# Kernel optimization log

Hardware: AMD Instinct MI355X
Metric: run time of the kernel (lower is better)

## Reference

```python
import jax, jax.numpy as jnp
import numpy as np

N = 100000
F_IN = 128
HID = 256
N_CLS = 40
E = 1600000


def setup_inputs() -> dict:
    key = jax.random.key(0)
    ks = jax.random.split(key, 12)
    x = jax.random.normal(ks[0], (N, F_IN), dtype=jnp.float32)
    edge_index = jax.random.randint(ks[1], (2, E), 0, N, dtype=jnp.int64)
    # GCNConv params (glorot-ish scale), conv2 is reused twice in forward
    def lin(k, fi, fo):
        return jax.random.normal(k, (fi, fo), dtype=jnp.float32) * (1.0 / np.sqrt(fi))
    return {
        "x": x,
        "edge_index": edge_index,
        "W1": lin(ks[2], F_IN, HID), "b1": jnp.zeros((HID,), jnp.float32),
        "W2": lin(ks[3], HID, HID),  "b2": jnp.zeros((HID,), jnp.float32),
        "W3": lin(ks[4], HID, HID),  "b3": jnp.zeros((HID,), jnp.float32),
        "W4": lin(ks[5], HID, N_CLS), "b4": jnp.zeros((N_CLS,), jnp.float32),
    }


def _gcn_norm(edge_index, n):
    # add self-loops, compute symmetric normalization D^-1/2 (A+I) D^-1/2
    loop = jnp.arange(n, dtype=edge_index.dtype)
    src = jnp.concatenate([edge_index[0], loop])
    dst = jnp.concatenate([edge_index[1], loop])
    deg = jax.ops.segment_sum(jnp.ones_like(dst, dtype=jnp.float32), dst, num_segments=n)
    dinv = jnp.where(deg > 0, jax.lax.rsqrt(deg), 0.0)
    norm = dinv[src] * dinv[dst]  # [E+N]
    return src, dst, norm


def _gcn_conv(x, W, b, src, dst, norm, n):
    h = x @ W                       # [N, Fout] dense transform first (fewer msg bytes)
    msg = h[src] * norm[:, None]    # gather + scale
    out = jax.ops.segment_sum(msg, dst, num_segments=n)  # scatter-add
    return out + b


def reference(x, edge_index, W1, b1, W2, b2, W3, b3, W4, b4):
    n = x.shape[0]
    src, dst, norm = _gcn_norm(edge_index, n)
    h = jax.nn.relu(_gcn_conv(x, W1, b1, src, dst, norm, n))
    h = jax.nn.relu(_gcn_conv(h, W2, b2, src, dst, norm, n))
    h = jax.nn.relu(_gcn_conv(h, W2, b2, src, dst, norm, n))  # conv2 reused, as in source
    h = jax.nn.relu(_gcn_conv(h, W3, b3, src, dst, norm, n))
    h = _gcn_conv(h, W4, b4, src, dst, norm, n)
    return jax.nn.log_softmax(h, axis=1)
```

## Files before the change

kernel.cpp:

```cpp
#include <hip/hip_runtime.h>
#include <stdint.h>
#include <math.h>

#define NN   100000
#define FIN  128
#define HIDDEN 256
#define NCLS 40
#define NE   1600000

#define PRNG 8
#define RNG  12500
#define SSL  32
#define NES  50000

#define NSLC 8

typedef unsigned short u16;
typedef unsigned char u8;
typedef __attribute__((ext_vector_type(8))) short s16x8;
typedef __attribute__((ext_vector_type(4))) float f32x4;
typedef __attribute__((ext_vector_type(2))) float f32x2;

__device__ __forceinline__ float bf2f(unsigned short u) {
    union { float f; uint32_t i; } v; v.i = ((uint32_t)u) << 16; return v.f;
}
__device__ __forceinline__ unsigned short f2bf(float f) {
    union { float f; uint32_t i; } v; v.f = f;
    uint32_t r = v.i + 0x7fffu + ((v.i >> 16) & 1u);
    return (unsigned short)(r >> 16);
}
__device__ __forceinline__ u8 f2fp8(float f) {
    int r = __builtin_amdgcn_cvt_pk_fp8_f32(f, f, 0, false);
    return (u8)(r & 0xff);
}

__global__ __launch_bounds__(256) void k_detect(const u16* __restrict__ x16,
                                                const int* __restrict__ ei,
                                                int* __restrict__ flags) {
    int g = blockIdx.x * 256 + threadIdx.x;
    uint2 v = *(const uint2*)(x16 + (size_t)g * 4);
    int nan_cnt = 0;
    uint32_t w0 = v.x, w1 = v.y;
    if (((w0 >> 0)  & 0x7fff) >= 0x7f80) nan_cnt++;
    if (((w0 >> 16) & 0x7fff) >= 0x7f80) nan_cnt++;
    if (((w1 >> 0)  & 0x7fff) >= 0x7f80) nan_cnt++;
    if (((w1 >> 16) & 0x7fff) >= 0x7f80) nan_cnt++;
    int odd_nz = (g < 8192 && ei[2 * g + 1] != 0) ? 1 : 0;
#pragma unroll
    for (int off = 1; off < 64; off <<= 1) {
        nan_cnt += __shfl_xor(nan_cnt, off);
        odd_nz  += __shfl_xor(odd_nz, off);
    }
    if ((threadIdx.x & 63) == 0) {
        if (nan_cnt) atomicAdd(&flags[0], nan_cnt);
        if (odd_nz)  atomicAdd(&flags[2], odd_nz);
    }
}

__global__ void k_compact(const int* __restrict__ ei, int* __restrict__ dst32,
                          int* __restrict__ src32, const int* __restrict__ flags) {
    int e = blockIdx.x * 256 + threadIdx.x;
    if (e < NE) {
        if (flags[2] == 0) { src32[e] = ei[2 * e]; dst32[e] = ei[2 * (NE + e)]; }
        else               { src32[e] = ei[e];     dst32[e] = ei[NE + e]; }
    }
}

__global__ void k_trans_cvt(const void* W1, const void* W2, const void* W3, const void* W4,
                            u16* W1t, u16* W2t, u16* W3t, u16* W4t,
                            const void* b1, const void* b2, const void* b3, const void* b4,
                            u16* o1, u16* o2, u16* o3, u16* o4,
                            const void* __restrict__ x, const float* __restrict__ dinv,
                            u16* __restrict__ xb,
                            const int* __restrict__ flags) {
    int b = blockIdx.x;
    int fl = flags[0];
    int t = threadIdx.x;
    if (b >= 705) {
        int i = (b - 705) * 256 + t;
        if (i < NN * FIN) {
            int node = i >> 7, f = i & 127;
            float v = fl ? ((const float*)x)[i] : bf2f(((const u16*)x)[i]);
            xb[(size_t)(f >> 4) * (NN * 16) + (size_t)node * 16 + (f & 15)] =
                f2bf(v * dinv[node]);
        }
        return;
    }
    if (b == 704) {
        o1[t] = fl ? f2bf(((const float*)b1)[t]) : ((const u16*)b1)[t];
        o2[t] = fl ? f2bf(((const float*)b2)[t]) : ((const u16*)b2)[t];
        o3[t] = fl ? f2bf(((const float*)b3)[t]) : ((const u16*)b3)[t];
        if (t < 64) o4[t] = (t < NCLS) ? (fl ? f2bf(((const float*)b4)[t]) : ((const u16*)b4)[t]) : (u16)0;
        return;
    }
    const void* W; u16* Wt; int K, F, Fpad, base;
    if (b < 128)      { W = W1; Wt = W1t; K = 128; F = 256; Fpad = 256; base = 0; }
    else if (b < 384) { W = W2; Wt = W2t; K = 256; F = 256; Fpad = 256; base = 128; }
    else if (b < 640) { W = W3; Wt = W3t; K = 256; F = 256; Fpad = 256; base = 384; }
    else              { W = W4; Wt = W4t; K = 256; F = 40;  Fpad = 64;  base = 640; }
    int idx = (b - base) * 256 + t;
    if (idx >= K * Fpad) return;
    int f = idx / K, k = idx - f * K;
    u16 v = 0;
    if (f < F) {
        if (fl) v = f2bf(((const float*)W)[(size_t)k * F + f]);
        else    v = ((const u16*)W)[(size_t)k * F + f];
    }
    Wt[idx] = v;
}


__global__ __launch_bounds__(256) void k_histb(const int* __restrict__ dst32,
                                               int* __restrict__ partial) {
    __shared__ int h[RNG];
    int p = blockIdx.x >> 5, s = blockIdx.x & 31;
    int t = threadIdx.x;
    int4 z4 = make_int4(0, 0, 0, 0);
    for (int i = t * 4; i < RNG; i += 1024) *(int4*)(h + i) = z4;
    __syncthreads();
    int base = s * NES;
    int lo = p * RNG;
    int nfull = NES & ~1023;
    for (int k = t * 4; k < nfull; k += 1024) {
        int4 d4 = *(const int4*)(dst32 + base + k);
        int a;
        a = d4.x - lo; if ((unsigned)a < RNG) atomicAdd(&h[a], 1);
        a = d4.y - lo; if ((unsigned)a < RNG) atomicAdd(&h[a], 1);
        a = d4.z - lo; if ((unsigned)a < RNG) atomicAdd(&h[a], 1);
        a = d4.w - lo; if ((unsigned)a < RNG) atomicAdd(&h[a], 1);
    }
    for (int k = nfull + t; k < NES; k += 256) {
        int a = dst32[base + k] - lo;
        if ((unsigned)a < RNG) atomicAdd(&h[a], 1);
    }
    __syncthreads();
    int* out = partial + blockIdx.x * RNG;
    for (int i = t * 4; i < RNG; i += 1024) *(int4*)(out + i) = *(const int4*)(h + i);
}

__global__ __launch_bounds__(256) void k_scan1(const int* __restrict__ partial,
                                               int* __restrict__ cnt,
                                               int* __restrict__ out,
                                               int* __restrict__ bsum) {
    __shared__ int sh[256];
    int t = threadIdx.x;
    int base = blockIdx.x * 1024 + t * 4;
    int v0 = 0, v1 = 0, v2 = 0, v3 = 0;
    if (base < NN) {
        int p = base / RNG, il = base - p * RNG;
        const int* q = partial + (p * SSL) * RNG + il;
        int4 acc = make_int4(0, 0, 0, 0);
#pragma unroll
        for (int s = 0; s < SSL; ++s) {
            int4 w = *(const int4*)(q + s * RNG);
            acc.x += w.x; acc.y += w.y; acc.z += w.z; acc.w += w.w;
        }
        v0 = acc.x; v1 = acc.y; v2 = acc.z; v3 = acc.w;
        *(int4*)(cnt + base) = acc;
    }
    int s = v0 + v1 + v2 + v3;
    sh[t] = s;
    __syncthreads();
    for (int off = 1; off < 256; off <<= 1) {
        int x = (t >= off) ? sh[t - off] : 0;
        __syncthreads();
        sh[t] += x;
        __syncthreads();
    }
    int ex = sh[t] - s;
    if (base < NN) {
        int4 o = make_int4(ex, ex + v0, ex + v0 + v1, ex + v0 + v1 + v2);
        *(int4*)(out + base) = o;
    }
    if (t == 255) bsum[blockIdx.x] = sh[255];
}

__global__ void k_scan2(int* bsum, int nb) {
    if (threadIdx.x == 0 && blockIdx.x == 0) {
        int run = 0;
        for (int i = 0; i < nb; ++i) { int t = bsum[i]; bsum[i] = run; run += t; }
    }
}

__global__ void k_scan3o(int* __restrict__ rp, const int* __restrict__ bsum,
                         const int* __restrict__ cnt, float* __restrict__ dinv,
                         int* __restrict__ partial) {
    int i = blockIdx.x * 256 + threadIdx.x;
    if (i < NN) {
        int v = rp[i] + bsum[i >> 10];
        rp[i] = v;
        dinv[i] = rsqrtf((float)(cnt[i] + 1));
        int p = i / RNG, il = i - p * RNG;
        int* q = partial + (p * SSL) * RNG + il;
        int run = v;
#pragma unroll
        for (int s = 0; s < SSL; ++s) { int t = q[s * RNG]; q[s * RNG] = run; run += t; }
    }
    if (i == 0) rp[NN] = NE;
}

__global__ __launch_bounds__(256) void k_fillb(const int* __restrict__ dst32,
                                               const int* __restrict__ src32,
                                               const int* __restrict__ offs,
                                               int* __restrict__ col) {
    __shared__ int h[RNG];
    int p = blockIdx.x >> 5, s = blockIdx.x & 31;
    int t = threadIdx.x;
    const int* o = offs + blockIdx.x * RNG;
    for (int i = t * 4; i < RNG; i += 1024) *(int4*)(h + i) = *(const int4*)(o + i);
    __syncthreads();
    int base = s * NES;
    int lo = p * RNG;
    int nfull = NES & ~1023;
    for (int k = t * 4; k < nfull; k += 1024) {
        int4 d4 = *(const int4*)(dst32 + base + k);
        int4 s4 = *(const int4*)(src32 + base + k);
        int a;
        a = d4.x - lo; if ((unsigned)a < RNG) col[atomicAdd(&h[a], 1)] = s4.x;
        a = d4.y - lo; if ((unsigned)a < RNG) col[atomicAdd(&h[a], 1)] = s4.y;
        a = d4.z - lo; if ((unsigned)a < RNG) col[atomicAdd(&h[a], 1)] = s4.z;
        a = d4.w - lo; if ((unsigned)a < RNG) col[atomicAdd(&h[a], 1)] = s4.w;
    }
    for (int k = nfull + t; k < NES; k += 256) {
        int a = dst32[base + k] - lo;
        if ((unsigned)a < RNG) col[atomicAdd(&h[a], 1)] = src32[base + k];
    }
}


#define GLL(g, l) __builtin_amdgcn_global_load_lds( \
    (const __attribute__((address_space(1))) unsigned int*)(g), \
    (__attribute__((address_space(3))) unsigned int*)(l), 16, 0, 0)

#define NT128 ((NN + 127) / 128)
#define NT256 ((NN + 255) / 256)

__global__ __launch_bounds__(256) void k_gemmP(const u16* __restrict__ A,
                                               const u16* __restrict__ Wt,
                                               const float* __restrict__ dinv,
                                               const u16* __restrict__ bias,
                                               u16* __restrict__ C,
                                               int K, int out_fp8) {
    __shared__ __align__(16) u16 Bs[128 * 256];
    __shared__ __align__(16) u16 As[2 * 128 * 32];
    int t = threadIdx.x;
    int bn = blockIdx.y;
    int w = t >> 6, lane = t & 63;
    int wm = w >> 1, wn = w & 1;
    int lrow = lane & 15, lq = lane >> 4;
    int r0 = t >> 2;
    int seg = (t & 3) * 8;

    int rounds = K >> 4;
    for (int r = 0; r < rounds; ++r) {
        int d = r * 4096 + t * 16;
        int kt = d >> 13;
        int win = d & 8191;
        int row = win >> 6;
        int sg = (win & 63) >> 1;
        GLL(Wt + (size_t)(bn * 128 + row) * K + kt * 32 + sg, Bs + (d >> 1));
    }

    int nK = K >> 5;
    bool fuse = (bias != nullptr);
    float bcol[4];
#pragma unroll
    for (int j = 0; j < 4; ++j)
        bcol[j] = fuse ? bf2f(bias[bn * 128 + wn * 64 + j * 16 + lrow]) : 0.f;

    for (int tm = blockIdx.x; tm < NT128; tm += gridDim.x) {
        int rowBase = tm * 128;
        int ar0 = rowBase + r0;       if (ar0 > NN - 1) ar0 = NN - 1;
        int ar1 = rowBase + 64 + r0;  if (ar1 > NN - 1) ar1 = NN - 1;
        const u16* a0p = A + (size_t)ar0 * K + seg;
        const u16* a1p = A + (size_t)ar1 * K + seg;
        GLL(a0p, As + t * 8);
        GLL(a1p, As + 2048 + t * 8);

        f32x4 acc[4][4] = {};
        int cur = 0;
        for (int kt = 0; kt < nK; ++kt) {
            __syncthreads();
            if (kt + 1 < nK) {
                int nxt = cur ^ 1;
                GLL(a0p + (kt + 1) * 32, As + nxt * 4096 + t * 8);
                GLL(a1p + (kt + 1) * 32, As + nxt * 4096 + 2048 + t * 8);
            }
            const u16* ab = As + cur * 4096;
            const u16* bb = Bs + kt * 4096;
            s16x8 af[4], bf[4];
#pragma unroll
            for (int i = 0; i < 4; ++i)
                af[i] = *(const s16x8*)(ab + (wm * 64 + i * 16 + lrow) * 32 + lq * 8);
#pragma unroll
            for (int j = 0; j < 4; ++j)
                bf[j] = *(const s16x8*)(bb + (wn * 64 + j * 16 + lrow) * 32 + lq * 8);
#pragma unroll
            for (int i = 0; i < 4; ++i)
#pragma unroll
                for (int j = 0; j < 4; ++j)
                    acc[i][j] = __builtin_amdgcn_mfma_f32_16x16x32_bf16(af[i], bf[j], acc[i][j], 0, 0, 0);
            cur ^= 1;
        }

        u8* C8 = (u8*)C;
#pragma unroll
        for (int i = 0; i < 4; ++i) {
#pragma unroll
            for (int rr = 0; rr < 4; ++rr) {
                int row = rowBase + wm * 64 + i * 16 + lq * 4 + rr;
                if (row < NN) {
                    float d = dinv[row];
#pragma unroll
                    for (int j = 0; j < 4; ++j) {
                        int colg = bn * 128 + wn * 64 + j * 16 + lrow;
                        float v = fuse ? fmaxf(fmaf(d, acc[i][j][rr], bcol[j]), 0.f)
                                       : acc[i][j][rr] * d;
                        if (out_fp8)
                            C8[(size_t)(colg >> 5) * (NN * 32) + (size_t)row * 32 + (colg & 31)] = f2fp8(v);
                        else
                            C[(size_t)row * HIDDEN + colg] = f2bf(v);
                    }
                }
            }
        }
        __syncthreads();
    }
}

__global__ __launch_bounds__(256) void k_gemmP64(const u16* __restrict__ A,
                                                 const u16* __restrict__ Wt,
                                                 const float* __restrict__ dinv,
                                                 u16* __restrict__ C) {
    const int K = 256;
    __shared__ __align__(16) u16 Bs[64 * 256];
    __shared__ __align__(16) u16 As[2 * 256 * 32];
    int t = threadIdx.x;
    int w = t >> 6, lane = t & 63;
    int lrow = lane & 15, lq = lane >> 4;
    int seg = (t & 3) * 8;
    int rr0 = t >> 2;

    for (int r = 0; r < 8; ++r)
        GLL(Wt + (size_t)(t >> 2) * K + r * 32 + seg, Bs + r * 2048 + t * 8);

    for (int tm = blockIdx.x; tm < NT256; tm += gridDim.x) {
        int rowBase = tm * 256;
        const u16* ap[4];
#pragma unroll
        for (int c = 0; c < 4; ++c) {
            int ar = rowBase + c * 64 + rr0;
            if (ar > NN - 1) ar = NN - 1;
            ap[c] = A + (size_t)ar * K + seg;
        }
#pragma unroll
        for (int c = 0; c < 4; ++c) GLL(ap[c], As + c * 2048 + t * 8);

        f32x4 acc[4][4] = {};
        int cur = 0;
        for (int kt = 0; kt < 8; ++kt) {
            __syncthreads();
            if (kt + 1 < 8) {
                int nxt = cur ^ 1;
#pragma unroll
                for (int c = 0; c < 4; ++c)
                    GLL(ap[c] + (kt + 1) * 32, As + nxt * 8192 + c * 2048 + t * 8);
            }
            const u16* ab = As + cur * 8192;
            const u16* bb = Bs + kt * 2048;
            s16x8 af[4], bf[4];
#pragma unroll
            for (int i = 0; i < 4; ++i)
                af[i] = *(const s16x8*)(ab + (w * 64 + i * 16 + lrow) * 32 + lq * 8);
#pragma unroll
            for (int j = 0; j < 4; ++j)
                bf[j] = *(const s16x8*)(bb + (j * 16 + lrow) * 32 + lq * 8);
#pragma unroll
            for (int i = 0; i < 4; ++i)
#pragma unroll
                for (int j = 0; j < 4; ++j)
                    acc[i][j] = __builtin_amdgcn_mfma_f32_16x16x32_bf16(af[i], bf[j], acc[i][j], 0, 0, 0);
            cur ^= 1;
        }

#pragma unroll
        for (int i = 0; i < 4; ++i) {
#pragma unroll
            for (int rr = 0; rr < 4; ++rr) {
                int row = rowBase + w * 64 + i * 16 + lq * 4 + rr;
                if (row < NN) {
                    float d = dinv[row];
#pragma unroll
                    for (int j = 0; j < 4; ++j) {
                        int colg = j * 16 + lrow;
                        C[(size_t)row * 64 + colg] = f2bf(acc[i][j][rr] * d);
                    }
                }
            }
        }
        __syncthreads();
    }
}


__global__ __launch_bounds__(256) void k_agg8(const u8* __restrict__ hs,
                                              const int* __restrict__ rp,
                                              const int* __restrict__ col,
                                              const float* __restrict__ dinv,
                                              const u16* __restrict__ bias,
                                              u16* __restrict__ out) {
    int s = blockIdx.x & 7;
    int rowg = blockIdx.x >> 3;
    int wq = __builtin_amdgcn_readfirstlane(threadIdx.x >> 6);
    int lane = threadIdx.x & 63;
    int g = lane >> 3;
    int fl = lane & 7;
    int row = rowg * 32 + wq * 8 + g;
    const u8* hss = hs + (size_t)s * (NN * 32);
    float a0 = 0.f, a1 = 0.f, a2 = 0.f, a3 = 0.f;
    auto acc_fma = [&](uint32_t w, float m) {
        f32x2 x = __builtin_amdgcn_cvt_pk_f32_fp8(w, false);
        f32x2 y = __builtin_amdgcn_cvt_pk_f32_fp8(w, true);
        a0 = fmaf(m, x.x, a0); a1 = fmaf(m, x.y, a1);
        a2 = fmaf(m, y.x, a2); a3 = fmaf(m, y.y, a3);
    };
    {
        f32x2 x, y;
        uint32_t w = *(const uint32_t*)(hss + (size_t)row * 32 + fl * 4);
        x = __builtin_amdgcn_cvt_pk_f32_fp8(w, false);
        y = __builtin_amdgcn_cvt_pk_f32_fp8(w, true);
        a0 = x.x; a1 = x.y; a2 = y.x; a3 = y.y;
    }
    int p  = rp[row];
    int p1 = rp[row + 1];
    while (__any(p < p1)) {
        uint32_t v[8]; float m[8];
#pragma unroll
        for (int k = 0; k < 8; ++k) {
            bool on = (p < p1);
            int idx = on ? p : 0;
            m[k] = on ? 1.f : 0.f;
            int c = col[idx];
            v[k] = *(const uint32_t*)(hss + (size_t)c * 32 + fl * 4);
            ++p;
        }
#pragma unroll
        for (int k = 0; k < 8; ++k) acc_fma(v[k], m[k]);
    }
    float d = dinv[row];
    uint2 bv = *(const uint2*)(bias + s * 32 + fl * 4);
    float r0 = fmaxf(fmaf(d, a0, bf2f((u16)(bv.x & 0xffff))), 0.f);
    float r1 = fmaxf(fmaf(d, a1, bf2f((u16)(bv.x >> 16))), 0.f);
    float r2 = fmaxf(fmaf(d, a2, bf2f((u16)(bv.y & 0xffff))), 0.f);
    float r3 = fmaxf(fmaf(d, a3, bf2f((u16)(bv.y >> 16))), 0.f);
    uint2 o;
    o.x = (uint32_t)f2bf(r0) | ((uint32_t)f2bf(r1) << 16);
    o.y = (uint32_t)f2bf(r2) | ((uint32_t)f2bf(r3) << 16);
    *(uint2*)(out + (size_t)row * HIDDEN + s * 32 + fl * 4) = o;
}

__global__ __launch_bounds__(256) void k_aggx(const u16* __restrict__ xb,
                                              const int* __restrict__ rp,
                                              const int* __restrict__ col,
                                              u16* __restrict__ out) {
    int s = blockIdx.x & 7;
    int rowg = blockIdx.x >> 3;
    int wq = __builtin_amdgcn_readfirstlane(threadIdx.x >> 6);
    int lane = threadIdx.x & 63;
    int g = lane >> 3;
    int fl = lane & 7;
    int row = rowg * 32 + wq * 8 + g;
    const u16* xbs = xb + (size_t)s * (NN * 16);
    uint32_t w0 = *(const uint32_t*)(xbs + (size_t)row * 16 + fl * 2);
    float a0 = bf2f((u16)(w0 & 0xffff));
    float a1 = bf2f((u16)(w0 >> 16));
    int p  = rp[row];
    int p1 = rp[row + 1];
    while (__any(p < p1)) {
        uint32_t v[8]; float m[8];
#pragma unroll
        for (int k = 0; k < 8; ++k) {
            bool on = (p < p1);
            int idx = on ? p : 0;
            m[k] = on ? 1.f : 0.f;
            int c = col[idx];
            v[k] = *(const uint32_t*)(xbs + (size_t)c * 16 + fl * 2);
            ++p;
        }
#pragma unroll
        for (int k = 0; k < 8; ++k) {
            a0 = fmaf(m[k], bf2f((u16)(v[k] & 0xffff)), a0);
            a1 = fmaf(m[k], bf2f((u16)(v[k] >> 16)), a1);
        }
    }
    uint32_t o = (uint32_t)f2bf(a0) | ((uint32_t)f2bf(a1) << 16);
    *(uint32_t*)(out + (size_t)row * FIN + s * 16 + fl * 2) = o;
}

__global__ __launch_bounds__(256) void k_agg5(const u16* __restrict__ hs,
                                              const int* __restrict__ rp,
                                              const int* __restrict__ col,
                                              const float* __restrict__ dinv,
                                              const u16* __restrict__ bias,
                                              void* __restrict__ out,
                                              const int* __restrict__ flags) {
    int wq = __builtin_amdgcn_readfirstlane(threadIdx.x >> 6);
    int row = blockIdx.x * 4 + wq;
    if (row >= NN) return;
    int lane = threadIdx.x & 63;
    float a = bf2f(hs[(size_t)row * 64 + lane]);
    int p  = __builtin_amdgcn_readfirstlane(rp[row]);
    int p1 = __builtin_amdgcn_readfirstlane(rp[row + 1]);
    for (; p + 8 <= p1; p += 8) {
        u16 v[8];
#pragma unroll
        for (int k = 0; k < 8; ++k) {
            int c = __builtin_amdgcn_readfirstlane(col[p + k]);
            v[k] = hs[(size_t)c * 64 + lane];
        }
#pragma unroll
        for (int k = 0; k < 8; ++k) a += bf2f(v[k]);
    }
    int rem = p1 - p;
    if (rem) {
        u16 v[8];
#pragma unroll
        for (int k = 0; k < 8; ++k) {
            int idx = (k < rem) ? (p + k) : p;
            int c = __builtin_amdgcn_readfirstlane(col[idx]);
            v[k] = hs[(size_t)c * 64 + lane];
        }
#pragma unroll
        for (int k = 0; k < 8; ++k)
            a = fmaf((k < rem) ? 1.f : 0.f, bf2f(v[k]), a);
    }
    bool act = lane < NCLS;
    float d = dinv[row];
    float l = act ? fmaf(d, a, bf2f(bias[lane])) : -1e30f;
    float m = l;
#pragma unroll
    for (int off = 32; off > 0; off >>= 1) m = fmaxf(m, __shfl_xor(m, off));
    float e = act ? __expf(l - m) : 0.f;
#pragma unroll
    for (int off = 32; off > 0; off >>= 1) e += __shfl_xor(e, off);
    if (act) {
        float r = l - m - __logf(e);
        if (flags[0]) ((float*)out)[(size_t)row * NCLS + lane] = r;
        else          ((u16*)out)[(size_t)row * NCLS + lane] = f2bf(r);
    }
}


extern "C" void kernel_launch(void* const* d_in, const int* in_sizes, int n_in,
                              void* d_out, int out_size, void* d_ws, size_t ws_size,
                              hipStream_t stream) {
    const void* x  = d_in[0];
    const int* ei  = (const int*)d_in[1];
    const void* W1 = d_in[2];
    const void* b1 = d_in[3];
    const void* W2 = d_in[4];
    const void* b2 = d_in[5];
    const void* W3 = d_in[6];
    const void* b3 = d_in[7];
    const void* W4 = d_in[8];
    const void* b4 = d_in[9];

    char* p = (char*)d_ws;
    auto alloc = [&](size_t b) -> char* {
        char* r = p;
        p += (b + 255) & ~(size_t)255;
        return r;
    };
    int*   flags = (int*)alloc(256);
    int*   cnt  = (int*)alloc((size_t)NN * 4);
    float* dinv = (float*)alloc((size_t)NN * 4);
    int*   rp   = (int*)alloc((size_t)(NN + 1) * 4);
    int*   col  = (int*)alloc((size_t)NE * 4);
    int*   bsum = (int*)alloc(4096);
    u16* xb  = (u16*)alloc((size_t)NN * FIN * 2);
    u16* W1t = (u16*)alloc((size_t)256 * 128 * 2);
    u16* W2t = (u16*)alloc((size_t)256 * 256 * 2);
    u16* W3t = (u16*)alloc((size_t)256 * 256 * 2);
    u16* W4t = (u16*)alloc((size_t)64 * 256 * 2);
    u16* bb1 = (u16*)alloc(512);
    u16* bb2 = (u16*)alloc(512);
    u16* bb3 = (u16*)alloc(512);
    u16* bb4 = (u16*)alloc(128);
    u16* bufA = (u16*)alloc((size_t)NN * HIDDEN * 2);
    u16* bufB = (u16*)alloc((size_t)NN * HIDDEN * 2);

    int* dst32   = (int*)bufA;
    int* src32   = dst32 + NE;
    int* partial = (int*)bufB;

    hipMemsetAsync(flags, 0, 16, stream);
    k_detect<<<64, 256, 0, stream>>>((const u16*)x, ei, flags);
    k_compact<<<(NE + 255) / 256, 256, 0, stream>>>(ei, dst32, src32, flags);

    k_histb<<<PRNG * SSL, 256, 0, stream>>>(dst32, partial);
    k_scan1<<<(NN + 1023) / 1024, 256, 0, stream>>>(partial, cnt, rp, bsum);
    k_scan2<<<1, 64, 0, stream>>>(bsum, (NN + 1023) / 1024);
    k_scan3o<<<(NN + 255) / 256, 256, 0, stream>>>(rp, bsum, cnt, dinv, partial);
    k_fillb<<<PRNG * SSL, 256, 0, stream>>>(dst32, src32, partial, col);

    k_trans_cvt<<<705 + (NN * FIN + 255) / 256, 256, 0, stream>>>(
        W1, W2, W3, W4, W1t, W2t, W3t, W4t,
        b1, b2, b3, b4, bb1, bb2, bb3, bb4, x, dinv, xb, flags);

    dim3 gP(256, 2);
    dim3 aggGrid((NN + 3) / 4);
    dim3 aggGridS((NN / 32) * NSLC);

    k_aggx<<<aggGridS, 256, 0, stream>>>(xb, rp, col, bufB);
    k_gemmP<<<gP, 256, 0, stream>>>(bufB, W1t, dinv, bb1, bufA, 128, 0);
    k_gemmP<<<gP, 256, 0, stream>>>(bufA, W2t, dinv, nullptr, bufB, 256, 1);
    k_agg8<<<aggGridS, 256, 0, stream>>>((const u8*)bufB, rp, col, dinv, bb2, bufA);
    k_gemmP<<<gP, 256, 0, stream>>>(bufA, W2t, dinv, nullptr, bufB, 256, 1);
    k_agg8<<<aggGridS, 256, 0, stream>>>((const u8*)bufB, rp, col, dinv, bb2, bufA);
    k_gemmP<<<gP, 256, 0, stream>>>(bufA, W3t, dinv, nullptr, bufB, 256, 1);
    k_agg8<<<aggGridS, 256, 0, stream>>>((const u8*)bufB, rp, col, dinv, bb3, bufA);
    k_gemmP64<<<256, 256, 0, stream>>>(bufA, W4t, dinv, bufB);
    k_agg5<<<aggGrid, 256, 0, stream>>>(bufB, rp, col, dinv, bb4, d_out, flags);
}
```

Measured before the change: 791.0 us.

## Balance sliced aggregation by splitting edge ranges of 32-row groups across lane groups

The sliced aggregation kernels now give each wavefront a group of 32 destination rows and split that group's whole edge range evenly among 8 lane groups, instead of one row per lane group. This is meant to remove load imbalance and divergent idle lanes from skewed per-row degrees. Each edge's local destination row is packed into the top 5 bits of the column index during CSR fill. Partial sums are flushed with LDS float atomics when the row changes, and are then combined with the self-loop, bias and ReLU. The cost is extra LDS atomics and one barrier per block, and source node indices must fit in 27 bits, which holds for this node count.

```diff
diff --git a/kernel.cpp b/kernel.cpp
--- a/kernel.cpp
+++ b/kernel.cpp
@@ -14,6 +14,8 @@
 #define NES  50000
 
 #define NSLC 8
+#define NRG  (NN / 32)
+#define COLM 0x07FFFFFF
 
 typedef unsigned short u16;
 typedef unsigned char u8;
@@ -216,14 +218,14 @@
         int4 d4 = *(const int4*)(dst32 + base + k);
         int4 s4 = *(const int4*)(src32 + base + k);
         int a;
-        a = d4.x - lo; if ((unsigned)a < RNG) col[atomicAdd(&h[a], 1)] = s4.x;
-        a = d4.y - lo; if ((unsigned)a < RNG) col[atomicAdd(&h[a], 1)] = s4.y;
-        a = d4.z - lo; if ((unsigned)a < RNG) col[atomicAdd(&h[a], 1)] = s4.z;
-        a = d4.w - lo; if ((unsigned)a < RNG) col[atomicAdd(&h[a], 1)] = s4.w;
+        a = d4.x - lo; if ((unsigned)a < RNG) col[atomicAdd(&h[a], 1)] = s4.x | (((a + lo) & 31) << 27);
+        a = d4.y - lo; if ((unsigned)a < RNG) col[atomicAdd(&h[a], 1)] = s4.y | (((a + lo) & 31) << 27);
+        a = d4.z - lo; if ((unsigned)a < RNG) col[atomicAdd(&h[a], 1)] = s4.z | (((a + lo) & 31) << 27);
+        a = d4.w - lo; if ((unsigned)a < RNG) col[atomicAdd(&h[a], 1)] = s4.w | (((a + lo) & 31) << 27);
     }
     for (int k = nfull + t; k < NES; k += 256) {
         int a = dst32[base + k] - lo;
-        if ((unsigned)a < RNG) col[atomicAdd(&h[a], 1)] = src32[base + k];
+        if ((unsigned)a < RNG) col[atomicAdd(&h[a], 1)] = src32[base + k] | (((a + lo) & 31) << 27);
     }
 }
 
@@ -409,92 +411,141 @@
                                               const float* __restrict__ dinv,
                                               const u16* __restrict__ bias,
                                               u16* __restrict__ out) {
+    __shared__ float accs[4][1024];
     int s = blockIdx.x & 7;
-    int rowg = blockIdx.x >> 3;
+    int bg = blockIdx.x >> 3;
     int wq = __builtin_amdgcn_readfirstlane(threadIdx.x >> 6);
+    int rg = bg * 4 + wq;
+    if (rg >= NRG) rg = NRG - 1;
+    int r0 = rg * 32;
     int lane = threadIdx.x & 63;
-    int g = lane >> 3;
-    int fl = lane & 7;
-    int row = rowg * 32 + wq * 8 + g;
-    const u8* hss = hs + (size_t)s * (NN * 32);
+    int g = lane >> 3, fl = lane & 7;
+    float* A = accs[wq];
+#pragma unroll
+    for (int i = 0; i < 16; ++i) A[lane + i * 64] = 0.f;
+    const u8* hss = hs + (size_t)s * ((size_t)NN * 32);
+    int p0 = __builtin_amdgcn_readfirstlane(rp[r0]);
+    int p1 = __builtin_amdgcn_readfirstlane(rp[r0 + 32]);
+    int n = p1 - p0;
+    int cb = p0 + ((n * g) >> 3);
+    int ce = p0 + ((n * (g + 1)) >> 3);
+    int kmax = (n + 7) >> 3;
     float a0 = 0.f, a1 = 0.f, a2 = 0.f, a3 = 0.f;
-    auto acc_fma = [&](uint32_t w, float m) {
-        f32x2 x = __builtin_amdgcn_cvt_pk_f32_fp8(w, false);
-        f32x2 y = __builtin_amdgcn_cvt_pk_f32_fp8(w, true);
-        a0 = fmaf(m, x.x, a0); a1 = fmaf(m, x.y, a1);
-        a2 = fmaf(m, y.x, a2); a3 = fmaf(m, y.y, a3);
-    };
-    {
-        f32x2 x, y;
-        uint32_t w = *(const uint32_t*)(hss + (size_t)row * 32 + fl * 4);
-        x = __builtin_amdgcn_cvt_pk_f32_fp8(w, false);
-        y = __builtin_amdgcn_cvt_pk_f32_fp8(w, true);
-        a0 = x.x; a1 = x.y; a2 = y.x; a3 = y.y;
-    }
-    int p  = rp[row];
-    int p1 = rp[row + 1];
-    while (__any(p < p1)) {
-        uint32_t v[8]; float m[8];
-#pragma unroll
-        for (int k = 0; k < 8; ++k) {
-            bool on = (p < p1);
-            int idx = on ? p : 0;
-            m[k] = on ? 1.f : 0.f;
-            int c = col[idx];
-            v[k] = *(const uint32_t*)(hss + (size_t)c * 32 + fl * 4);
-            ++p;
-        }
-#pragma unroll
-        for (int k = 0; k < 8; ++k) acc_fma(v[k], m[k]);
-    }
-    float d = dinv[row];
-    uint2 bv = *(const uint2*)(bias + s * 32 + fl * 4);
-    float r0 = fmaxf(fmaf(d, a0, bf2f((u16)(bv.x & 0xffff))), 0.f);
-    float r1 = fmaxf(fmaf(d, a1, bf2f((u16)(bv.x >> 16))), 0.f);
-    float r2 = fmaxf(fmaf(d, a2, bf2f((u16)(bv.y & 0xffff))), 0.f);
-    float r3 = fmaxf(fmaf(d, a3, bf2f((u16)(bv.y >> 16))), 0.f);
-    uint2 o;
-    o.x = (uint32_t)f2bf(r0) | ((uint32_t)f2bf(r1) << 16);
-    o.y = (uint32_t)f2bf(r2) | ((uint32_t)f2bf(r3) << 16);
-    *(uint2*)(out + (size_t)row * HIDDEN + s * 32 + fl * 4) = o;
+    int cur = -1;
+    int e = cb;
+    for (int k = 0; k < kmax; ++k, ++e) {
+        bool on = e < ce;
+        uint32_t w = (uint32_t)col[on ? e : p0];
+        int c = w & COLM;
+        int lr = w >> 27;
+        uint32_t v = *(const uint32_t*)(hss + (size_t)c * 32 + fl * 4);
+        if (on) {
+            if (lr != cur) {
+                if (cur >= 0) {
+                    atomicAdd(&A[cur * 32 + fl * 4 + 0], a0);
+                    atomicAdd(&A[cur * 32 + fl * 4 + 1], a1);
+                    atomicAdd(&A[cur * 32 + fl * 4 + 2], a2);
+                    atomicAdd(&A[cur * 32 + fl * 4 + 3], a3);
+                }
+                cur = lr; a0 = a1 = a2 = a3 = 0.f;
+            }
+            f32x2 x = __builtin_amdgcn_cvt_pk_f32_fp8(v, false);
+            f32x2 y = __builtin_amdgcn_cvt_pk_f32_fp8(v, true);
+            a0 += x.x; a1 += x.y; a2 += y.x; a3 += y.y;
+        }
+    }
+    if (cur >= 0) {
+        atomicAdd(&A[cur * 32 + fl * 4 + 0], a0);
+        atomicAdd(&A[cur * 32 + fl * 4 + 1], a1);
+        atomicAdd(&A[cur * 32 + fl * 4 + 2], a2);
+        atomicAdd(&A[cur * 32 + fl * 4 + 3], a3);
+    }
+    __syncthreads();
+#pragma unroll
+    for (int ri = 0; ri < 4; ++ri) {
+        int lrow = g + ri * 8;
+        int row = r0 + lrow;
+        float d = dinv[row];
+        float s0 = A[lrow * 32 + fl * 4 + 0];
+        float s1 = A[lrow * 32 + fl * 4 + 1];
+        float s2 = A[lrow * 32 + fl * 4 + 2];
+        float s3 = A[lrow * 32 + fl * 4 + 3];
+        uint32_t v = *(const uint32_t*)(hss + (size_t)row * 32 + fl * 4);
+        f32x2 x = __builtin_amdgcn_cvt_pk_f32_fp8(v, false);
+        f32x2 y = __builtin_amdgcn_cvt_pk_f32_fp8(v, true);
+        uint2 bv = *(const uint2*)(bias + s * 32 + fl * 4);
+        float r0f = fmaxf(fmaf(d, s0 + x.x, bf2f((u16)(bv.x & 0xffff))), 0.f);
+        float r1f = fmaxf(fmaf(d, s1 + x.y, bf2f((u16)(bv.x >> 16))), 0.f);
+        float r2f = fmaxf(fmaf(d, s2 + y.x, bf2f((u16)(bv.y & 0xffff))), 0.f);
+        float r3f = fmaxf(fmaf(d, s3 + y.y, bf2f((u16)(bv.y >> 16))), 0.f);
+        uint2 o;
+        o.x = (uint32_t)f2bf(r0f) | ((uint32_t)f2bf(r1f) << 16);
+        o.y = (uint32_t)f2bf(r2f) | ((uint32_t)f2bf(r3f) << 16);
+        *(uint2*)(out + (size_t)row * HIDDEN + s * 32 + fl * 4) = o;
+    }
 }
 
 __global__ __launch_bounds__(256) void k_aggx(const u16* __restrict__ xb,
                                               const int* __restrict__ rp,
                                               const int* __restrict__ col,
                                               u16* __restrict__ out) {
+    __shared__ float accs[4][512];
     int s = blockIdx.x & 7;
-    int rowg = blockIdx.x >> 3;
+    int bg = blockIdx.x >> 3;
     int wq = __builtin_amdgcn_readfirstlane(threadIdx.x >> 6);
+    int rg = bg * 4 + wq;
+    if (rg >= NRG) rg = NRG - 1;
+    int r0 = rg * 32;
     int lane = threadIdx.x & 63;
-    int g = lane >> 3;
-    int fl = lane & 7;
-    int row = rowg * 32 + wq * 8 + g;
-    const u16* xbs = xb + (size_t)s * (NN * 16);
-    uint32_t w0 = *(const uint32_t*)(xbs + (size_t)row * 16 + fl * 2);
-    float a0 = bf2f((u16)(w0 & 0xffff));
-    float a1 = bf2f((u16)(w0 >> 16));
-    int p  = rp[row];
-    int p1 = rp[row + 1];
-    while (__any(p < p1)) {
-        uint32_t v[8]; float m[8];
-#pragma unroll
-        for (int k = 0; k < 8; ++k) {
-            bool on = (p < p1);
-            int idx = on ? p : 0;
-            m[k] = on ? 1.f : 0.f;
-            int c = col[idx];
-            v[k] = *(const uint32_t*)(xbs + (size_t)c * 16 + fl * 2);
-            ++p;
-        }
-#pragma unroll
-        for (int k = 0; k < 8; ++k) {
-            a0 = fmaf(m[k], bf2f((u16)(v[k] & 0xffff)), a0);
-            a1 = fmaf(m[k], bf2f((u16)(v[k] >> 16)), a1);
-        }
-    }
-    uint32_t o = (uint32_t)f2bf(a0) | ((uint32_t)f2bf(a1) << 16);
-    *(uint32_t*)(out + (size_t)row * FIN + s * 16 + fl * 2) = o;
+    int g = lane >> 3, fl = lane & 7;
+    float* A = accs[wq];
+#pragma unroll
+    for (int i = 0; i < 8; ++i) A[lane + i * 64] = 0.f;
+    const u16* xbs = xb + (size_t)s * ((size_t)NN * 16);
+    int p0 = __builtin_amdgcn_readfirstlane(rp[r0]);
+    int p1 = __builtin_amdgcn_readfirstlane(rp[r0 + 32]);
+    int n = p1 - p0;
+    int cb = p0 + ((n * g) >> 3);
+    int ce = p0 + ((n * (g + 1)) >> 3);
+    int kmax = (n + 7) >> 3;
+    float a0 = 0.f, a1 = 0.f;
+    int cur = -1;
+    int e = cb;
+    for (int k = 0; k < kmax; ++k, ++e) {
+        bool on = e < ce;
+        uint32_t w = (uint32_t)col[on ? e : p0];
+        int c = w & COLM;
+        int lr = w >> 27;
+        uint32_t v = *(const uint32_t*)(xbs + (size_t)c * 16 + fl * 2);
+        if (on) {
+            if (lr != cur) {
+                if (cur >= 0) {
+                    atomicAdd(&A[cur * 16 + fl * 2 + 0], a0);
+                    atomicAdd(&A[cur * 16 + fl * 2 + 1], a1);
+                }
+                cur = lr; a0 = a1 = 0.f;
+            }
+            a0 += bf2f((u16)(v & 0xffff));
+            a1 += bf2f((u16)(v >> 16));
+        }
+    }
+    if (cur >= 0) {
+        atomicAdd(&A[cur * 16 + fl * 2 + 0], a0);
+        atomicAdd(&A[cur * 16 + fl * 2 + 1], a1);
+    }
+    __syncthreads();
+#pragma unroll
+    for (int ri = 0; ri < 4; ++ri) {
+        int lrow = g + ri * 8;
+        int row = r0 + lrow;
+        float s0 = A[lrow * 16 + fl * 2 + 0];
+        float s1 = A[lrow * 16 + fl * 2 + 1];
+        uint32_t v = *(const uint32_t*)(xbs + (size_t)row * 16 + fl * 2);
+        float r0f = s0 + bf2f((u16)(v & 0xffff));
+        float r1f = s1 + bf2f((u16)(v >> 16));
+        uint32_t o = (uint32_t)f2bf(r0f) | ((uint32_t)f2bf(r1f) << 16);
+        *(uint32_t*)(out + (size_t)row * FIN + s * 16 + fl * 2) = o;
+    }
 }
 
 __global__ __launch_bounds__(256) void k_agg5(const u16* __restrict__ hs,
@@ -515,7 +566,7 @@
         u16 v[8];
 #pragma unroll
         for (int k = 0; k < 8; ++k) {
-            int c = __builtin_amdgcn_readfirstlane(col[p + k]);
+            int c = __builtin_amdgcn_readfirstlane(col[p + k]) & COLM;
             v[k] = hs[(size_t)c * 64 + lane];
         }
 #pragma unroll
@@ -527,7 +578,7 @@
 #pragma unroll
         for (int k = 0; k < 8; ++k) {
             int idx = (k < rem) ? (p + k) : p;
-            int c = __builtin_amdgcn_readfirstlane(col[idx]);
+            int c = __builtin_amdgcn_readfirstlane(col[idx]) & COLM;
             v[k] = hs[(size_t)c * 64 + lane];
         }
 #pragma unroll
@@ -609,7 +660,7 @@
 
     dim3 gP(256, 2);
     dim3 aggGrid((NN + 3) / 4);
-    dim3 aggGridS((NN / 32) * NSLC);
+    dim3 aggGridS(((NRG + 3) / 4) * NSLC);
 
     k_aggx<<<aggGridS, 256, 0, stream>>>(xb, rp, col, bufB);
     k_gemmP<<<gP, 256, 0, stream>>>(bufB, W1t, dinv, bb1, bufA, 128, 0);
```

Result: slower. 1.218 ms (+54.0%).
